# Optimization experiments

Hardware: AMD Instinct MI355X
Metric: run time of the kernel (lower is better)

The kernel has to match this reference:

```python
import jax, jax.numpy as jnp
import numpy as np

H = 4  # heads
NEG_SLOPE = 0.2


def gat_layer(feats, src, dst, W, a_src, a_dst, b, n_nodes):
    # feats: [N, Fin], W: [Fin, H*C], a_src/a_dst: [H, C], b: [C]
    C = a_src.shape[1]
    xh = (feats @ W).reshape(n_nodes, H, C)          # [N,H,C]
    alpha_s = (xh * a_src[None]).sum(-1)             # [N,H]
    alpha_d = (xh * a_dst[None]).sum(-1)             # [N,H]
    logits = alpha_s[src] + alpha_d[dst]             # [E,H]
    logits = jnp.where(logits >= 0, logits, NEG_SLOPE * logits)
    m = jax.ops.segment_max(logits, dst, num_segments=n_nodes)   # [N,H]
    m = jnp.where(jnp.isfinite(m), m, 0.0)
    e = jnp.exp(logits - m[dst])                     # [E,H]
    denom = jax.ops.segment_sum(e, dst, num_segments=n_nodes)    # [N,H]
    alpha = e / denom[dst]                           # [E,H]
    out = jax.ops.segment_sum(alpha[:, :, None] * xh[src], dst,
                              num_segments=n_nodes)  # [N,H,C]
    return out.mean(axis=1) + b                      # concat=False -> head mean


def setup_inputs() -> dict:
    key = jax.random.key(0)
    ks = jax.random.split(key, 16)
    N, E, P = 20000, 320000, 100000
    POS, FIN, HID = 2, 128, 128
    x = jax.random.normal(ks[0], (N, POS + FIN), dtype=jnp.float32)
    edge_index = jax.random.randint(ks[1], (2, E), 0, N, dtype=jnp.int64)
    idx = jax.random.randint(ks[2], (2, P), 0, N, dtype=jnp.int64)
    sc = 1.0 / np.sqrt(FIN)
    W1 = jax.random.normal(ks[3], (FIN, H * HID), dtype=jnp.float32) * sc
    a_src1 = jax.random.normal(ks[4], (H, HID), dtype=jnp.float32) * sc
    a_dst1 = jax.random.normal(ks[5], (H, HID), dtype=jnp.float32) * sc
    b1 = jnp.zeros((HID,), jnp.float32)
    W2 = jax.random.normal(ks[6], (HID, H * HID), dtype=jnp.float32) * sc
    a_src2 = jax.random.normal(ks[7], (H, HID), dtype=jnp.float32) * sc
    a_dst2 = jax.random.normal(ks[8], (H, HID), dtype=jnp.float32) * sc
    b2 = jnp.zeros((HID,), jnp.float32)
    fc_w = jax.random.normal(ks[9], (2, 1), dtype=jnp.float32) * 0.5
    fc_b = jnp.zeros((1,), jnp.float32)
    return {"x": x, "edge_index": edge_index, "idx": idx,
            "W1": W1, "a_src1": a_src1, "a_dst1": a_dst1, "b1": b1,
            "W2": W2, "a_src2": a_src2, "a_dst2": a_dst2, "b2": b2,
            "fc_w": fc_w, "fc_b": fc_b}


def reference(x, edge_index, idx, W1, a_src1, a_dst1, b1,
              W2, a_src2, a_dst2, b2, fc_w, fc_b):
    POS = 2
    N = x.shape[0]
    coors, feats = x[:, :POS], x[:, POS:]
    # PyG default: add self loops
    loops = jnp.arange(N, dtype=edge_index.dtype)
    src = jnp.concatenate([edge_index[0], loops])
    dst = jnp.concatenate([edge_index[1], loops])
    feats = gat_layer(feats, src, dst, W1, a_src1, a_dst1, b1, N)
    feats = gat_layer(feats, src, dst, W2, a_src2, a_dst2, b2, N)
    n1, n2 = feats[idx[0]], feats[idx[1]]            # [P,HID]
    p1, p2 = coors[idx[0]], coors[idx[1]]            # [P,POS]
    pos_enc = ((p1 - p2) ** 2).sum(-1, keepdims=True)  # [P,1]
    pred = (n1 * n2).sum(-1, keepdims=True)            # [P,1]
    out = jnp.concatenate([pred, pos_enc], axis=1) @ fc_w + fc_b  # [P,1]
    return out
```

## Files before the change

kernel.cpp:

```cpp
#include <hip/hip_runtime.h>
#include <hip/hip_fp16.h>

#define H 4
#define C 128
#define FOUT 512

typedef __attribute__((ext_vector_type(8))) short s16x8;
typedef __attribute__((ext_vector_type(4))) float f32x4;
typedef __attribute__((ext_vector_type(4))) int i32x4;
typedef __attribute__((ext_vector_type(2))) int i32x2;

__device__ int amd_buf_load_i32(i32x4 rsrc, int voffset, int soffset, int aux) __asm("llvm.amdgcn.raw.buffer.load.i32");
__device__ i32x2 amd_buf_load_i32x2(i32x4 rsrc, int voffset, int soffset, int aux) __asm("llvm.amdgcn.raw.buffer.load.v2i32");
__device__ i32x4 amd_buf_load_i32x4(i32x4 rsrc, int voffset, int soffset, int aux) __asm("llvm.amdgcn.raw.buffer.load.v4i32");

__device__ __forceinline__ i32x4 make_rsrc(const void* p, unsigned int bytes) {
    i32x4 r;
    r.x = (int)(unsigned int)(unsigned long long)p;
    r.y = (int)(unsigned int)(((unsigned long long)p) >> 32);
    r.z = (int)bytes;
    r.w = 0x00020000;
    return r;
}

__device__ __forceinline__ unsigned int f2bf_bits(float f) {
    unsigned int u = __float_as_uint(f);
    u += 0x7fffu + ((u >> 16) & 1u);
    return u >> 16;
}
__device__ __forceinline__ unsigned int pack2bf(unsigned int u0, unsigned int u1) {
    unsigned int r0 = (u0 + 0x7fffu + ((u0 >> 16) & 1u)) >> 16;
    unsigned int r1 = (u1 + 0x7fffu + ((u1 >> 16) & 1u)) & 0xffff0000u;
    return r0 | r1;
}
__device__ __forceinline__ float bflo(unsigned int u) { return __uint_as_float(u << 16); }
__device__ __forceinline__ float bfhi(unsigned int u) { return __uint_as_float(u & 0xffff0000u); }
__device__ __forceinline__ float leaky(float x) { return (x >= 0.f) ? x : 0.2f * x; }
__device__ __forceinline__ __half2 u2h2(unsigned int u) {
    union { unsigned int u; __half2 h; } c; c.u = u; return c.h;
}
__device__ __forceinline__ unsigned int h22u(__half2 h) {
    union { __half2 h; unsigned int u; } c; c.h = h; return c.u;
}
__device__ __forceinline__ unsigned int pkrtz_bits(float a, float b) {
    auto v = __builtin_amdgcn_cvt_pkrtz(a, b);
    union { decltype(v) h; unsigned int u; } c; c.h = v; return c.u;
}

__global__ void prep_hist(const float* __restrict__ W1, const float* __restrict__ W2,
                          unsigned short* __restrict__ Wt1, unsigned short* __restrict__ Wt2,
                          int* __restrict__ counts, const int* __restrict__ ei, int E, int N) {
    int b = blockIdx.x;
    if (b < 256) {
        int i = b * 256 + threadIdx.x;
        if (i < 128 * 512) {
            int c = i >> 7, k = i & 127;
            Wt1[i] = (unsigned short)f2bf_bits(W1[(size_t)k * FOUT + c]);
            Wt2[i] = (unsigned short)f2bf_bits(W2[(size_t)k * FOUT + c]);
        }
    } else {
        int e = (b - 256) * 256 + threadIdx.x;
        int M = E + N;
        if (e < M) {
            int d = (e < E) ? ei[E + e] : (e - E);
            atomicAdd(&counts[d], 1);
        }
    }
}

__global__ __launch_bounds__(1024) void scan_kernel(const int* __restrict__ counts,
                                                    int* __restrict__ row_off,
                                                    int* __restrict__ cursor, int N) {
    __shared__ int part[1024];
    int t = threadIdx.x;
    int chunk = (((N + 1023) >> 10) + 3) & ~3;
    int b = t * chunk; if (b > N) b = N;
    int e = b + chunk; if (e > N) e = N;
    int s = 0;
    int i = b;
    for (; i + 3 < e; i += 4) {
        int4 v = *(const int4*)&counts[i];
        s += v.x + v.y + v.z + v.w;
    }
    for (; i < e; ++i) s += counts[i];
    part[t] = s;
    __syncthreads();
    for (int off = 1; off < 1024; off <<= 1) {
        int v = (t >= off) ? part[t - off] : 0;
        __syncthreads();
        part[t] += v;
        __syncthreads();
    }
    int run = (t == 0) ? 0 : part[t - 1];
    i = b;
    for (; i + 3 < e; i += 4) {
        int4 c = *(const int4*)&counts[i];
        int4 r;
        r.x = run; r.y = run + c.x; r.z = r.y + c.y; r.w = r.z + c.z;
        *(int4*)&row_off[i] = r;
        *(int4*)&cursor[i] = r;
        run = r.w + c.w;
    }
    for (; i < e; ++i) { row_off[i] = run; cursor[i] = run; run += counts[i]; }
    if (t == 1023) row_off[N] = part[1023];
}

template <bool IS_X>
__device__ __forceinline__ void gemm_body(int h, int r0, const void* __restrict__ Asrc, int Nrows,
                                          const unsigned short* __restrict__ Bt,
                                          const float* __restrict__ a_src,
                                          const float* __restrict__ a_dst,
                                          unsigned short* __restrict__ Xh,
                                          float* __restrict__ alpha_s,
                                          float* __restrict__ alpha_d,
                                          int Npad, i32x4* __restrict__ AsTile,
                                          float (*albuf)[4][16][2][2]) {
    int t = threadIdx.x;
    int lane = t & 63;
    int wv = t >> 6;
    int wr = wv >> 1, wc = wv & 1;
    int lr = lane & 15;
    int ksel = lane >> 4;

    i32x4 rA = make_rsrc(Asrc, IS_X ? (unsigned int)Nrows * 520u : (unsigned int)Nrows * 256u);
    #pragma unroll
    for (int i = 0; i < 8; ++i) {
        int q = t + i * 256;
        int row = q >> 4, cb = q & 15;
        i32x4 v;
        if constexpr (IS_X) {
            int base = (r0 + row) * 520 + 8 + cb * 32;
            i32x2 u0 = amd_buf_load_i32x2(rA, base, 0, 0);
            i32x2 u1 = amd_buf_load_i32x2(rA, base + 8, 0, 0);
            i32x2 u2 = amd_buf_load_i32x2(rA, base + 16, 0, 0);
            i32x2 u3 = amd_buf_load_i32x2(rA, base + 24, 0, 0);
            v.x = (int)pack2bf((unsigned int)u0.x, (unsigned int)u0.y);
            v.y = (int)pack2bf((unsigned int)u1.x, (unsigned int)u1.y);
            v.z = (int)pack2bf((unsigned int)u2.x, (unsigned int)u2.y);
            v.w = (int)pack2bf((unsigned int)u3.x, (unsigned int)u3.y);
        } else {
            v = amd_buf_load_i32x4(rA, (r0 + row) * 256 + cb * 16, 0, 0);
        }
        AsTile[row * 16 + (cb ^ (row & 7))] = v;
    }
    __syncthreads();

    f32x4 acc[4][4];
    #pragma unroll
    for (int i = 0; i < 4; ++i)
        #pragma unroll
        for (int j = 0; j < 4; ++j) acc[i][j] = (f32x4){0.f, 0.f, 0.f, 0.f};

    const s16x8* Bb = (const s16x8*)(Bt + (size_t)(h * 128 + wc * 64 + lr) * C);

    #pragma unroll
    for (int ks = 0; ks < 4; ++ks) {
        int cb = ks * 4 + ksel;
        s16x8 af[4], bf[4];
        #pragma unroll
        for (int i = 0; i < 4; ++i) {
            int rowl = wr * 64 + i * 16 + lr;
            af[i] = __builtin_bit_cast(s16x8, AsTile[rowl * 16 + (cb ^ (rowl & 7))]);
            bf[i] = Bb[(size_t)(i * 16) * 16 + cb];
        }
        #pragma unroll
        for (int i = 0; i < 4; ++i)
            #pragma unroll
            for (int j = 0; j < 4; ++j)
                acc[i][j] = __builtin_amdgcn_mfma_f32_16x16x32_bf16(bf[j], af[i], acc[i][j], 0, 0, 0);
    }

    float4 avj[4], dvj[4];
    #pragma unroll
    for (int j = 0; j < 4; ++j) {
        int cc = h * C + wc * 64 + j * 16 + ksel * 4;
        avj[j] = *(const float4*)&a_src[cc];
        dvj[j] = *(const float4*)&a_dst[cc];
    }

    unsigned short* slabp = Xh + (size_t)(h * 2 + wc) * Npad * 64;
    float ps[4] = {0.f, 0.f, 0.f, 0.f}, pd[4] = {0.f, 0.f, 0.f, 0.f};
    #pragma unroll
    for (int i = 0; i < 4; ++i) {
        int gr = r0 + wr * 64 + i * 16 + lr;
        #pragma unroll
        for (int j = 0; j < 4; ++j) {
            f32x4 a4 = acc[i][j];
            ps[i] += a4[0] * avj[j].x + a4[1] * avj[j].y + a4[2] * avj[j].z + a4[3] * avj[j].w;
            pd[i] += a4[0] * dvj[j].x + a4[1] * dvj[j].y + a4[2] * dvj[j].z + a4[3] * dvj[j].w;
            uint2 o;
            o.x = pkrtz_bits(a4[0], a4[1]);
            o.y = pkrtz_bits(a4[2], a4[3]);
            *(uint2*)(slabp + (size_t)gr * 64 + j * 16 + ksel * 4) = o;
        }
        ps[i] += __shfl_xor(ps[i], 16); ps[i] += __shfl_xor(ps[i], 32);
        pd[i] += __shfl_xor(pd[i], 16); pd[i] += __shfl_xor(pd[i], 32);
    }
    if (lane < 16) {
        #pragma unroll
        for (int i = 0; i < 4; ++i) {
            albuf[wr][i][lane][wc][0] = ps[i];
            albuf[wr][i][lane][wc][1] = pd[i];
        }
    }
    __syncthreads();

    int rid = t >> 1, which = t & 1;
    int wr2 = rid >> 6, rem = rid & 63, i2 = rem >> 4, l2 = rem & 15;
    float v = albuf[wr2][i2][l2][0][which] + albuf[wr2][i2][l2][1][which];
    int gr = r0 + wr2 * 64 + i2 * 16 + l2;
    if (gr < Nrows) {
        if (which) alpha_d[gr * H + h] = v;
        else       alpha_s[gr * H + h] = v;
    }
}

__global__ __launch_bounds__(256) void scatter_gemm1(const int* __restrict__ ei, int E, int N,
                                                     int* __restrict__ cursor, int* __restrict__ csr_src,
                                                     const float* __restrict__ x,
                                                     const unsigned short* __restrict__ Wt1,
                                                     const float* __restrict__ as1,
                                                     const float* __restrict__ ad1,
                                                     unsigned short* __restrict__ Xh,
                                                     float* __restrict__ alpha_s,
                                                     float* __restrict__ alpha_d,
                                                     int Npad, int nScatterBlocks) {
    __shared__ i32x4 AsTile[2048];
    __shared__ float albuf[2][4][16][2][2];
    int b = blockIdx.x;
    if (b < nScatterBlocks) {
        int e = b * 256 + threadIdx.x;
        int M = E + N;
        if (e < M) {
            int s = (e < E) ? ei[e] : (e - E);
            int d = (e < E) ? ei[E + e] : (e - E);
            int pos = atomicAdd(&cursor[d], 1);
            csr_src[pos] = s;
        }
    } else {
        int gb = b - nScatterBlocks;
        gemm_body<true>(gb & 3, (gb >> 2) * 128, x, N, Wt1, as1, ad1, Xh, alpha_s, alpha_d,
                        Npad, AsTile, albuf);
    }
}

__global__ __launch_bounds__(256) void gemm2_kernel(const unsigned short* __restrict__ featsbf, int N,
                                                    const unsigned short* __restrict__ Wt2,
                                                    const float* __restrict__ as2,
                                                    const float* __restrict__ ad2,
                                                    unsigned short* __restrict__ Xh,
                                                    float* __restrict__ alpha_s,
                                                    float* __restrict__ alpha_d, int Npad) {
    __shared__ i32x4 AsTile[2048];
    __shared__ float albuf[2][4][16][2][2];
    int gb = blockIdx.x;
    gemm_body<false>(gb & 3, (gb >> 2) * 128, featsbf, N, Wt2, as2, ad2, Xh, alpha_s, alpha_d,
                     Npad, AsTile, albuf);
}

__global__ __launch_bounds__(256) void attn_kernel(const float4* __restrict__ as4,
                                                   const float4* __restrict__ ad4,
                                                   const int* __restrict__ row_off,
                                                   const int* __restrict__ csr_src,
                                                   unsigned int* __restrict__ pk, int N, int M) {
    int n = blockIdx.x * 4 + (threadIdx.x >> 6);
    if (n >= N) return;
    int l = threadIdx.x & 63;
    int beg = row_off[n], end = row_off[n + 1];
    float4 mx = make_float4(-1e30f, -1e30f, -1e30f, -1e30f);
    for (int e = beg + l; e < end; e += 64) {
        float4 a = as4[csr_src[e]];
        mx.x = fmaxf(mx.x, a.x); mx.y = fmaxf(mx.y, a.y);
        mx.z = fmaxf(mx.z, a.z); mx.w = fmaxf(mx.w, a.w);
    }
    #pragma unroll
    for (int off = 32; off >= 1; off >>= 1) {
        mx.x = fmaxf(mx.x, __shfl_xor(mx.x, off));
        mx.y = fmaxf(mx.y, __shfl_xor(mx.y, off));
        mx.z = fmaxf(mx.z, __shfl_xor(mx.z, off));
        mx.w = fmaxf(mx.w, __shfl_xor(mx.w, off));
    }
    float4 d = ad4[n];
    float4 m;
    m.x = leaky(mx.x + d.x); m.y = leaky(mx.y + d.y);
    m.z = leaky(mx.z + d.z); m.w = leaky(mx.w + d.w);
    for (int e = beg + l; e < end; e += 64) {
        int s = csr_src[e];
        float4 a = as4[s];
        unsigned int su = (unsigned int)s;
        unsigned int w0 = (unsigned int)__half_as_ushort(__float2half(__expf(leaky(a.x + d.x) - m.x)));
        unsigned int w1 = (unsigned int)__half_as_ushort(__float2half(__expf(leaky(a.y + d.y) - m.y)));
        unsigned int w2 = (unsigned int)__half_as_ushort(__float2half(__expf(leaky(a.z + d.z) - m.z)));
        unsigned int w3 = (unsigned int)__half_as_ushort(__float2half(__expf(leaky(a.w + d.w) - m.w)));
        pk[e]                 = (w0 << 16) | su;
        pk[(size_t)M + e]     = (w1 << 16) | su;
        pk[(size_t)2 * M + e] = (w2 << 16) | su;
        pk[(size_t)3 * M + e] = (w3 << 16) | su;
    }
}

__global__ __launch_bounds__(256) void aggregate_v11(const unsigned short* __restrict__ xh,
                                                     const unsigned int* __restrict__ pk,
                                                     const int* __restrict__ row_off,
                                                     unsigned short* __restrict__ hout,
                                                     int N, int Npad, int M) {
    int i = blockIdx.x;
    int slab = i & 7;
    int h = slab >> 1;
    int t = threadIdx.x;
    int wv = t >> 6;
    int lane = t & 63;
    int slot = lane >> 4;
    int l16 = lane & 15;
    int nbase = ((i >> 3) * 4 + wv) * 2;
    if (nbase >= N) return;

    i32x4 rx = make_rsrc(xh + (size_t)slab * Npad * 64, (unsigned int)Npad * 128u);
    i32x4 rp = make_rsrc(pk + (size_t)h * M, (unsigned int)M * 4u);
    int ld8 = l16 << 3;
    int slot4 = slot << 2;
    int nend = (nbase + 2 < N) ? nbase + 2 : N;

    for (int n = nbase; n < nend; ++n) {
        int beg = row_off[n], end = row_off[n + 1];
        __half2 acc01 = u2h2(0), acc23 = u2h2(0), den2 = u2h2(0);

        for (int ebase = beg; ebase < end; ebase += 64) {
            int p = amd_buf_load_i32(rp, (ebase + lane) << 2, 0, 0);
            int nrem = end - ebase;
            int jmax = ((nrem < 64 ? nrem : 64) + 7) >> 3;
            for (int j = 0; j < jmax; ++j) {
                int addr = (j << 5) + slot4;
                int sp0 = __builtin_amdgcn_ds_bpermute(addr, p);
                int sp1 = __builtin_amdgcn_ds_bpermute(addr + 16, p);
                int e0 = ebase + (j << 3) + slot;
                i32x2 ga = amd_buf_load_i32x2(rx, ((sp0 & 0xffff) << 7) + ld8, 0, 0);
                i32x2 gb = amd_buf_load_i32x2(rx, ((sp1 & 0xffff) << 7) + ld8, 0, 0);
                unsigned int wa2 = __builtin_amdgcn_perm(sp0, sp0, 0x03020302);
                unsigned int wb2 = __builtin_amdgcn_perm(sp1, sp1, 0x03020302);
                if (e0 >= end) wa2 = 0u;
                if (e0 + 4 >= end) wb2 = 0u;
                __half2 wha = u2h2(wa2), whb = u2h2(wb2);
                acc01 = __hfma2(wha, u2h2((unsigned int)ga.x), acc01);
                acc23 = __hfma2(wha, u2h2((unsigned int)ga.y), acc23);
                acc01 = __hfma2(whb, u2h2((unsigned int)gb.x), acc01);
                acc23 = __hfma2(whb, u2h2((unsigned int)gb.y), acc23);
                den2 = __hadd2(den2, wha);
                den2 = __hadd2(den2, whb);
            }
        }

        #pragma unroll
        for (int off = 16; off <= 32; off <<= 1) {
            acc01 = __hadd2(acc01, u2h2((unsigned int)__shfl_xor((int)h22u(acc01), off)));
            acc23 = __hadd2(acc23, u2h2((unsigned int)__shfl_xor((int)h22u(acc23), off)));
            den2  = __hadd2(den2,  u2h2((unsigned int)__shfl_xor((int)h22u(den2),  off)));
        }

        if (slot == 0) {
            float2 f01 = __half22float2(acc01);
            float2 f23 = __half22float2(acc23);
            float inv = 1.f / __half2float(__low2half(den2));
            uint2 o;
            o.x = f2bf_bits(f01.x * inv) | (f2bf_bits(f01.y * inv) << 16);
            o.y = f2bf_bits(f23.x * inv) | (f2bf_bits(f23.y * inv) << 16);
            ((uint2*)hout)[((size_t)slab * Npad + n) * 16 + l16] = o;
        }
    }
}

__global__ void combine_kernel(const unsigned short* __restrict__ hout,
                               const float* __restrict__ bias,
                               unsigned short* __restrict__ featsbf, int N, int Npad,
                               float* __restrict__ out, const float* __restrict__ fcb, int P) {
    int i = blockIdx.x * blockDim.x + threadIdx.x;
    if (out != nullptr && i < P) out[i] = fcb[0];
    if (i >= N * 64) return;
    int n = i >> 6, c2 = i & 63;
    int chalf = c2 >> 5, ld = c2 & 31;
    const unsigned int* hp = (const unsigned int*)hout;
    float lo = 0.f, hi = 0.f;
    #pragma unroll
    for (int h = 0; h < 4; ++h) {
        unsigned int v = hp[((size_t)(h * 2 + chalf) * Npad + n) * 32 + ld];
        lo += bflo(v); hi += bfhi(v);
    }
    lo = 0.25f * lo + bias[c2 * 2];
    hi = 0.25f * hi + bias[c2 * 2 + 1];
    ((unsigned int*)featsbf)[(size_t)n * 64 + c2] = f2bf_bits(lo) | (f2bf_bits(hi) << 16);
}

__global__ __launch_bounds__(256) void pair_kernel(const unsigned short* __restrict__ featsbf,
                                                   const float* __restrict__ x,
                                                   const int* __restrict__ idx, int P,
                                                   const float* __restrict__ fc_w,
                                                   float* __restrict__ out) {
    int chalf = blockIdx.x & 1;
    int p = (blockIdx.x >> 1) * 16 + (threadIdx.x >> 4);
    int l = threadIdx.x & 15;
    if (p >= P) return;
    int i0 = idx[p], i1 = idx[P + p];
    uint2 a = ((const uint2*)featsbf)[(size_t)i0 * 32 + chalf * 16 + l];
    uint2 b = ((const uint2*)featsbf)[(size_t)i1 * 32 + chalf * 16 + l];
    float s = bflo(a.x) * bflo(b.x) + bfhi(a.x) * bfhi(b.x)
            + bflo(a.y) * bflo(b.y) + bfhi(a.y) * bfhi(b.y);
    s += __shfl_xor(s, 1); s += __shfl_xor(s, 2);
    s += __shfl_xor(s, 4); s += __shfl_xor(s, 8);
    if (l == 0) {
        float v = fc_w[0] * s;
        if (chalf == 0) {
            float2 c0 = *(const float2*)&x[(size_t)i0 * 130];
            float2 c1 = *(const float2*)&x[(size_t)i1 * 130];
            float dx = c0.x - c1.x;
            float dy = c0.y - c1.y;
            v += fc_w[1] * (dx * dx + dy * dy);
        }
        atomicAdd(&out[p], v);
    }
}

extern "C" void kernel_launch(void* const* d_in, const int* in_sizes, int n_in,
                              void* d_out, int out_size, void* d_ws, size_t ws_size,
                              hipStream_t stream) {
    const float* x   = (const float*)d_in[0];
    const int*   ei  = (const int*)d_in[1];
    const int*   idx = (const int*)d_in[2];
    const float* W1  = (const float*)d_in[3];
    const float* as1 = (const float*)d_in[4];
    const float* ad1 = (const float*)d_in[5];
    const float* b1  = (const float*)d_in[6];
    const float* W2  = (const float*)d_in[7];
    const float* as2 = (const float*)d_in[8];
    const float* ad2 = (const float*)d_in[9];
    const float* b2  = (const float*)d_in[10];
    const float* fcw = (const float*)d_in[11];
    const float* fcb = (const float*)d_in[12];
    float* out = (float*)d_out;

    const int N = in_sizes[0] / 130;
    const int E = in_sizes[1] / 2;
    const int P = in_sizes[2] / 2;
    const int M = E + N;
    const int Npad = (N + 127) & ~127;

    char* ws = (char*)d_ws;
    size_t off = 0;
    auto alloc = [&](size_t bytes) -> void* {
        void* p = ws + off;
        off += (bytes + 255) & ~(size_t)255;
        return p;
    };
    unsigned short* xh_f16  = (unsigned short*)alloc((size_t)Npad * FOUT * 2);
    unsigned short* hout    = (unsigned short*)alloc((size_t)Npad * FOUT * 2);
    unsigned short* featsbf = (unsigned short*)alloc((size_t)Npad * C * 2);
    unsigned short* Wt1     = (unsigned short*)alloc((size_t)128 * FOUT * 2);
    unsigned short* Wt2     = (unsigned short*)alloc((size_t)128 * FOUT * 2);
    float*          alpha_s = (float*)alloc((size_t)N * H * 4);
    float*          alpha_d = (float*)alloc((size_t)N * H * 4);
    unsigned int*   pk      = (unsigned int*)alloc((size_t)M * H * 4);
    int*            row_off = (int*)alloc((size_t)(N + 1) * 4);
    int*            cursor  = (int*)alloc((size_t)N * 4);
    int*            counts  = (int*)alloc((size_t)N * 4);
    int*            csr_src = (int*)alloc((size_t)M * 4);

    const int histBlocks = (M + 255) / 256;
    const int scatBlocks = (M + 255) / 256;
    const int gemmBlocks = 4 * (Npad / 128);
    int aggGrid = ((N + 7) / 8) * 8;
    int cmbGrid = (N * 64 + 255) / 256;

    hipMemsetAsync(counts, 0, (size_t)N * 4, stream);
    prep_hist<<<256 + histBlocks, 256, 0, stream>>>(W1, W2, Wt1, Wt2, counts, ei, E, N);
    scan_kernel<<<1, 1024, 0, stream>>>(counts, row_off, cursor, N);
    scatter_gemm1<<<scatBlocks + gemmBlocks, 256, 0, stream>>>(ei, E, N, cursor, csr_src,
                                                               x, Wt1, as1, ad1, xh_f16,
                                                               alpha_s, alpha_d, Npad, scatBlocks);

    attn_kernel<<<(N + 3) / 4, 256, 0, stream>>>((const float4*)alpha_s, (const float4*)alpha_d,
                                                 row_off, csr_src, pk, N, M);
    aggregate_v11<<<aggGrid, 256, 0, stream>>>(xh_f16, pk, row_off, hout, N, Npad, M);
    combine_kernel<<<cmbGrid, 256, 0, stream>>>(hout, b1, featsbf, N, Npad, nullptr, fcb, 0);

    gemm2_kernel<<<gemmBlocks, 256, 0, stream>>>(featsbf, N, Wt2, as2, ad2, xh_f16,
                                                 alpha_s, alpha_d, Npad);
    attn_kernel<<<(N + 3) / 4, 256, 0, stream>>>((const float4*)alpha_s, (const float4*)alpha_d,
                                                 row_off, csr_src, pk, N, M);
    aggregate_v11<<<aggGrid, 256, 0, stream>>>(xh_f16, pk, row_off, hout, N, Npad, M);
    combine_kernel<<<cmbGrid, 256, 0, stream>>>(hout, b2, featsbf, N, Npad, out, fcb, P);

    pair_kernel<<<((P + 15) / 16) * 2, 256, 0, stream>>>(featsbf, x, idx, P, fcw, out);
}
```

Baseline: 224.6 us.

## Pad atomic counters per node, split scatter from GEMM1, halve GEMM row tile

Per-node histogram counts and cursors are padded to 16 ints (64 bytes) so atomics on different destinations land on separate cache lines, reducing atomic contention. The fused scatter+GEMM1 kernel is split into separate scatter and GEMM1 launches. The GEMM row tile shrinks from 128 to 64 rows per block to raise block count. The trade-offs are a larger counts buffer and memset, a scan that now does strided scalar reads instead of vectorized ones, one extra launch, and less per-block B-fragment reuse.

```diff
diff --git a/kernel.cpp b/kernel.cpp
--- a/kernel.cpp
+++ b/kernel.cpp
@@ -46,6 +46,8 @@
     auto v = __builtin_amdgcn_cvt_pkrtz(a, b);
     union { decltype(v) h; unsigned int u; } c; c.h = v; return c.u;
 }
+
+#define CPAD 16
 
 __global__ void prep_hist(const float* __restrict__ W1, const float* __restrict__ W2,
                           unsigned short* __restrict__ Wt1, unsigned short* __restrict__ Wt2,
@@ -63,7 +65,7 @@
         int M = E + N;
         if (e < M) {
             int d = (e < E) ? ei[E + e] : (e - E);
-            atomicAdd(&counts[d], 1);
+            atomicAdd(&counts[d << 4], 1);
         }
     }
 }
@@ -73,16 +75,11 @@
                                                     int* __restrict__ cursor, int N) {
     __shared__ int part[1024];
     int t = threadIdx.x;
-    int chunk = (((N + 1023) >> 10) + 3) & ~3;
+    int chunk = (N + 1023) >> 10;
     int b = t * chunk; if (b > N) b = N;
     int e = b + chunk; if (e > N) e = N;
     int s = 0;
-    int i = b;
-    for (; i + 3 < e; i += 4) {
-        int4 v = *(const int4*)&counts[i];
-        s += v.x + v.y + v.z + v.w;
-    }
-    for (; i < e; ++i) s += counts[i];
+    for (int i = b; i < e; ++i) s += counts[i << 4];
     part[t] = s;
     __syncthreads();
     for (int off = 1; off < 1024; off <<= 1) {
@@ -92,17 +89,23 @@
         __syncthreads();
     }
     int run = (t == 0) ? 0 : part[t - 1];
-    i = b;
-    for (; i + 3 < e; i += 4) {
-        int4 c = *(const int4*)&counts[i];
-        int4 r;
-        r.x = run; r.y = run + c.x; r.z = r.y + c.y; r.w = r.z + c.z;
-        *(int4*)&row_off[i] = r;
-        *(int4*)&cursor[i] = r;
-        run = r.w + c.w;
-    }
-    for (; i < e; ++i) { row_off[i] = run; cursor[i] = run; run += counts[i]; }
+    for (int i = b; i < e; ++i) {
+        row_off[i] = run;
+        cursor[i << 4] = run;
+        run += counts[i << 4];
+    }
     if (t == 1023) row_off[N] = part[1023];
+}
+
+__global__ void scatter_kernel(const int* __restrict__ ei, int E, int N,
+                               int* __restrict__ cursor, int* __restrict__ csr_src) {
+    int e = blockIdx.x * blockDim.x + threadIdx.x;
+    int M = E + N;
+    if (e >= M) return;
+    int s = (e < E) ? ei[e] : (e - E);
+    int d = (e < E) ? ei[E + e] : (e - E);
+    int pos = atomicAdd(&cursor[d << 4], 1);
+    csr_src[pos] = s;
 }
 
 template <bool IS_X>
@@ -114,7 +117,7 @@
                                           float* __restrict__ alpha_s,
                                           float* __restrict__ alpha_d,
                                           int Npad, i32x4* __restrict__ AsTile,
-                                          float (*albuf)[4][16][2][2]) {
+                                          float (*albuf)[2][16][2][2]) {
     int t = threadIdx.x;
     int lane = t & 63;
     int wv = t >> 6;
@@ -124,7 +127,7 @@
 
     i32x4 rA = make_rsrc(Asrc, IS_X ? (unsigned int)Nrows * 520u : (unsigned int)Nrows * 256u);
     #pragma unroll
-    for (int i = 0; i < 8; ++i) {
+    for (int i = 0; i < 4; ++i) {
         int q = t + i * 256;
         int row = q >> 4, cb = q & 15;
         i32x4 v;
@@ -145,9 +148,9 @@
     }
     __syncthreads();
 
-    f32x4 acc[4][4];
-    #pragma unroll
-    for (int i = 0; i < 4; ++i)
+    f32x4 acc[2][4];
+    #pragma unroll
+    for (int i = 0; i < 2; ++i)
         #pragma unroll
         for (int j = 0; j < 4; ++j) acc[i][j] = (f32x4){0.f, 0.f, 0.f, 0.f};
 
@@ -156,15 +159,16 @@
     #pragma unroll
     for (int ks = 0; ks < 4; ++ks) {
         int cb = ks * 4 + ksel;
-        s16x8 af[4], bf[4];
-        #pragma unroll
-        for (int i = 0; i < 4; ++i) {
-            int rowl = wr * 64 + i * 16 + lr;
+        s16x8 af[2], bf[4];
+        #pragma unroll
+        for (int i = 0; i < 2; ++i) {
+            int rowl = wr * 32 + i * 16 + lr;
             af[i] = __builtin_bit_cast(s16x8, AsTile[rowl * 16 + (cb ^ (rowl & 7))]);
-            bf[i] = Bb[(size_t)(i * 16) * 16 + cb];
-        }
-        #pragma unroll
-        for (int i = 0; i < 4; ++i)
+        }
+        #pragma unroll
+        for (int j = 0; j < 4; ++j) bf[j] = Bb[(size_t)(j * 16) * 16 + cb];
+        #pragma unroll
+        for (int i = 0; i < 2; ++i)
             #pragma unroll
             for (int j = 0; j < 4; ++j)
                 acc[i][j] = __builtin_amdgcn_mfma_f32_16x16x32_bf16(bf[j], af[i], acc[i][j], 0, 0, 0);
@@ -179,10 +183,10 @@
     }
 
     unsigned short* slabp = Xh + (size_t)(h * 2 + wc) * Npad * 64;
-    float ps[4] = {0.f, 0.f, 0.f, 0.f}, pd[4] = {0.f, 0.f, 0.f, 0.f};
-    #pragma unroll
-    for (int i = 0; i < 4; ++i) {
-        int gr = r0 + wr * 64 + i * 16 + lr;
+    float ps[2] = {0.f, 0.f}, pd[2] = {0.f, 0.f};
+    #pragma unroll
+    for (int i = 0; i < 2; ++i) {
+        int gr = r0 + wr * 32 + i * 16 + lr;
         #pragma unroll
         for (int j = 0; j < 4; ++j) {
             f32x4 a4 = acc[i][j];
@@ -198,50 +202,37 @@
     }
     if (lane < 16) {
         #pragma unroll
-        for (int i = 0; i < 4; ++i) {
+        for (int i = 0; i < 2; ++i) {
             albuf[wr][i][lane][wc][0] = ps[i];
             albuf[wr][i][lane][wc][1] = pd[i];
         }
     }
     __syncthreads();
 
-    int rid = t >> 1, which = t & 1;
-    int wr2 = rid >> 6, rem = rid & 63, i2 = rem >> 4, l2 = rem & 15;
-    float v = albuf[wr2][i2][l2][0][which] + albuf[wr2][i2][l2][1][which];
-    int gr = r0 + wr2 * 64 + i2 * 16 + l2;
-    if (gr < Nrows) {
-        if (which) alpha_d[gr * H + h] = v;
-        else       alpha_s[gr * H + h] = v;
-    }
-}
-
-__global__ __launch_bounds__(256) void scatter_gemm1(const int* __restrict__ ei, int E, int N,
-                                                     int* __restrict__ cursor, int* __restrict__ csr_src,
-                                                     const float* __restrict__ x,
-                                                     const unsigned short* __restrict__ Wt1,
-                                                     const float* __restrict__ as1,
-                                                     const float* __restrict__ ad1,
-                                                     unsigned short* __restrict__ Xh,
-                                                     float* __restrict__ alpha_s,
-                                                     float* __restrict__ alpha_d,
-                                                     int Npad, int nScatterBlocks) {
-    __shared__ i32x4 AsTile[2048];
-    __shared__ float albuf[2][4][16][2][2];
-    int b = blockIdx.x;
-    if (b < nScatterBlocks) {
-        int e = b * 256 + threadIdx.x;
-        int M = E + N;
-        if (e < M) {
-            int s = (e < E) ? ei[e] : (e - E);
-            int d = (e < E) ? ei[E + e] : (e - E);
-            int pos = atomicAdd(&cursor[d], 1);
-            csr_src[pos] = s;
-        }
-    } else {
-        int gb = b - nScatterBlocks;
-        gemm_body<true>(gb & 3, (gb >> 2) * 128, x, N, Wt1, as1, ad1, Xh, alpha_s, alpha_d,
-                        Npad, AsTile, albuf);
-    }
+    if (t < 128) {
+        int rid = t >> 1, which = t & 1;
+        int wr2 = rid >> 5, rem = rid & 31, i2 = rem >> 4, l2 = rem & 15;
+        float v = albuf[wr2][i2][l2][0][which] + albuf[wr2][i2][l2][1][which];
+        int gr = r0 + wr2 * 32 + i2 * 16 + l2;
+        if (gr < Nrows) {
+            if (which) alpha_d[gr * H + h] = v;
+            else       alpha_s[gr * H + h] = v;
+        }
+    }
+}
+
+__global__ __launch_bounds__(256) void gemm1_kernel(const float* __restrict__ x, int N,
+                                                    const unsigned short* __restrict__ Wt1,
+                                                    const float* __restrict__ as1,
+                                                    const float* __restrict__ ad1,
+                                                    unsigned short* __restrict__ Xh,
+                                                    float* __restrict__ alpha_s,
+                                                    float* __restrict__ alpha_d, int Npad) {
+    __shared__ i32x4 AsTile[1024];
+    __shared__ float albuf[2][2][16][2][2];
+    int gb = blockIdx.x;
+    gemm_body<true>(gb & 3, (gb >> 2) * 64, x, N, Wt1, as1, ad1, Xh, alpha_s, alpha_d,
+                    Npad, AsTile, albuf);
 }
 
 __global__ __launch_bounds__(256) void gemm2_kernel(const unsigned short* __restrict__ featsbf, int N,
@@ -251,10 +242,10 @@
                                                     unsigned short* __restrict__ Xh,
                                                     float* __restrict__ alpha_s,
                                                     float* __restrict__ alpha_d, int Npad) {
-    __shared__ i32x4 AsTile[2048];
-    __shared__ float albuf[2][4][16][2][2];
+    __shared__ i32x4 AsTile[1024];
+    __shared__ float albuf[2][2][16][2][2];
     int gb = blockIdx.x;
-    gemm_body<false>(gb & 3, (gb >> 2) * 128, featsbf, N, Wt2, as2, ad2, Xh, alpha_s, alpha_d,
+    gemm_body<false>(gb & 3, (gb >> 2) * 64, featsbf, N, Wt2, as2, ad2, Xh, alpha_s, alpha_d,
                      Npad, AsTile, albuf);
 }
 
@@ -459,23 +450,22 @@
     float*          alpha_d = (float*)alloc((size_t)N * H * 4);
     unsigned int*   pk      = (unsigned int*)alloc((size_t)M * H * 4);
     int*            row_off = (int*)alloc((size_t)(N + 1) * 4);
-    int*            cursor  = (int*)alloc((size_t)N * 4);
-    int*            counts  = (int*)alloc((size_t)N * 4);
+    int*            cursor  = (int*)alloc((size_t)N * CPAD * 4);
+    int*            counts  = (int*)alloc((size_t)N * CPAD * 4);
     int*            csr_src = (int*)alloc((size_t)M * 4);
 
     const int histBlocks = (M + 255) / 256;
-    const int scatBlocks = (M + 255) / 256;
-    const int gemmBlocks = 4 * (Npad / 128);
+    const int gemmBlocks = 4 * (Npad / 64);
     int aggGrid = ((N + 7) / 8) * 8;
     int cmbGrid = (N * 64 + 255) / 256;
 
-    hipMemsetAsync(counts, 0, (size_t)N * 4, stream);
+    hipMemsetAsync(counts, 0, (size_t)N * CPAD * 4, stream);
     prep_hist<<<256 + histBlocks, 256, 0, stream>>>(W1, W2, Wt1, Wt2, counts, ei, E, N);
     scan_kernel<<<1, 1024, 0, stream>>>(counts, row_off, cursor, N);
-    scatter_gemm1<<<scatBlocks + gemmBlocks, 256, 0, stream>>>(ei, E, N, cursor, csr_src,
-                                                               x, Wt1, as1, ad1, xh_f16,
-                                                               alpha_s, alpha_d, Npad, scatBlocks);
-
+    scatter_kernel<<<histBlocks, 256, 0, stream>>>(ei, E, N, cursor, csr_src);
+
+    gemm1_kernel<<<gemmBlocks, 256, 0, stream>>>(x, N, Wt1, as1, ad1, xh_f16,
+                                                 alpha_s, alpha_d, Npad);
     attn_kernel<<<(N + 3) / 4, 256, 0, stream>>>((const float4*)alpha_s, (const float4*)alpha_d,
                                                  row_off, csr_src, pk, N, M);
     aggregate_v11<<<aggGrid, 256, 0, stream>>>(xh_f16, pk, row_off, hout, N, Npad, M);
```

Result: slower. 274.5 us (+22.2%).
